# Kernel tuning notes

Hardware: AMD Instinct MI355X
Metric: run time of the kernel (lower is better)

The kernel has to match this reference:

```python
import jax, jax.numpy as jnp
import numpy as np

IN_CH = 32
OUT_CH = 32
HIDDEN = 32  # edge/angle MLP hidden width


def setup_inputs() -> dict:
    key = jax.random.key(0)
    ks = jax.random.split(key, 13)
    N, E, A = 50000, 200000, 400000
    s = 0.1
    return {
        "x": jax.random.normal(ks[0], (N, IN_CH), dtype=jnp.float32),
        "edge_index": jax.random.randint(ks[1], (2, E), 0, N),
        "edge_attr": jax.random.uniform(ks[2], (E, 1), dtype=jnp.float32),
        "angle_index": jax.random.randint(ks[3], (3, A), 0, N),
        "angles": jax.random.uniform(ks[4], (A, 1), dtype=jnp.float32),
        # edge_mlp: Linear(1,32) -> ReLU -> Linear(32, in*out)
        "eW1": jax.random.normal(ks[5], (1, HIDDEN), dtype=jnp.float32) * s,
        "eb1": jax.random.normal(ks[6], (HIDDEN,), dtype=jnp.float32) * s,
        "eW2": jax.random.normal(ks[7], (HIDDEN, IN_CH * OUT_CH), dtype=jnp.float32) * s,
        "eb2": jax.random.normal(ks[8], (IN_CH * OUT_CH,), dtype=jnp.float32) * s,
        # angle_mlp: Linear(1,32) -> ReLU -> Linear(32, out)
        "aW1": jax.random.normal(ks[9], (1, HIDDEN), dtype=jnp.float32) * s,
        "ab1": jax.random.normal(ks[10], (HIDDEN,), dtype=jnp.float32) * s,
        "aW2": jax.random.normal(ks[11], (HIDDEN, OUT_CH), dtype=jnp.float32) * s,
        "ab2": jax.random.normal(ks[12], (OUT_CH,), dtype=jnp.float32) * s,
    }


def reference(x, edge_index, edge_attr, angle_index, angles,
              eW1, eb1, eW2, eb2, aW1, ab1, aW2, ab2):
    N = x.shape[0]
    row, col = edge_index[0], edge_index[1]
    # per-edge weight matrices from edge MLP: (E, in, out)
    h = jax.nn.relu(edge_attr @ eW1 + eb1)
    edge_w = (h @ eW2 + eb2).reshape(-1, IN_CH, OUT_CH)
    # gather source node features, apply per-edge matrix (bmm)
    msg = jnp.einsum('ei,eio->eo', x[col], edge_w)  # (E, out)
    agg = jax.ops.segment_sum(msg, row, num_segments=N)
    # angle branch: scatter angle features onto center node j
    j = angle_index[1]
    angle_feat = jax.nn.relu(angles @ aW1 + ab1) @ aW2 + ab2  # (A, out)
    agg = agg + jax.ops.segment_sum(angle_feat, j, num_segments=N)
    return agg
```

## Files before the change

### kernel.cpp

```cpp
#include <hip/hip_runtime.h>
#include <hip/hip_bf16.h>
#include <stdint.h>

#define IC 32
#define OC 32
#define HID 32

#define PBIN 16
#define TSH 44
#define TSCALE 1048576.0f

#define PBE 12
#define MAXN 65536

typedef __attribute__((ext_vector_type(8))) _Float16 half8;
typedef __attribute__((ext_vector_type(4))) float f32x4;
typedef unsigned long long u64;

static __device__ __forceinline__ _Float16 f2h(float f) { return (_Float16)f; }

__device__ __align__(16) _Float16 g_MK[PBE * 2 * 32 * 32];
__device__ float g_ekn[16];
__device__ float g_akn[16];
__device__ int   g_npc[2];
__device__ __align__(16) u64 g_cells[(size_t)MAXN * PBIN];

__global__ __launch_bounds__(512) void setup_zero(
    const float* __restrict__ eW1, const float* __restrict__ eb1,
    const float* __restrict__ eW2, const float* __restrict__ eb2,
    const float* __restrict__ aW1, const float* __restrict__ ab1,
    float* __restrict__ out, int outF4, int cellF4)
{
    __shared__ float ts_s[32];
    __shared__ int   rk_s[32];
    __shared__ int   re_s[32];
    const int tid = threadIdx.x;
    const int bid = blockIdx.x;

    if (bid < 48) {
        if (bid == 0 && tid < 16) { g_ekn[tid] = 1e30f; g_akn[tid] = 1e30f; }
        if (tid < 32) {
            const int k = tid;
            const float w = eW1[k], b = eb1[k];
            const float ts = -b / w;
            const bool re = (w != 0.f) && (ts > 0.f) && (ts < 1.f);
            int rk = 0;
            for (int k2 = 0; k2 < 32; ++k2) {
                const float w2 = eW1[k2], b2 = eb1[k2];
                const float t2 = -b2 / w2;
                const bool re2 = (w2 != 0.f) && (t2 > 0.f) && (t2 < 1.f);
                rk += (re2 && (t2 < ts || (t2 == ts && k2 < k))) ? 1 : 0;
            }
            ts_s[k] = ts; rk_s[k] = rk; re_s[k] = re ? 1 : 0;
        }
        __syncthreads();

        if (bid == 0) {
            if (tid < 32) {
                if (re_s[tid]) g_ekn[rk_s[tid]] = ts_s[tid];
                if (tid == 0) {
                    int n = 0;
                    for (int k = 0; k < 32; ++k) n += re_s[k];
                    g_npc[0] = n + 1;
                }
            } else if (tid < 64) {
                const int k = tid - 32;
                const float w = aW1[k], b = ab1[k];
                const float ts = -b / w;
                const bool re = (w != 0.f) && (ts > 0.f) && (ts < 1.f);
                int rk = 0, nre = 0;
                for (int k2 = 0; k2 < 32; ++k2) {
                    const float w2 = aW1[k2], b2 = ab1[k2];
                    const float t2 = -b2 / w2;
                    const bool re2 = (w2 != 0.f) && (t2 > 0.f) && (t2 < 1.f);
                    nre += re2 ? 1 : 0;
                    rk += (re2 && (t2 < ts || (t2 == ts && k2 < k))) ? 1 : 0;
                }
                if (re) g_akn[rk] = ts;
                if (k == 0) g_npc[1] = nre + 1;
            }
        }

        const int gid = bid * 512 + tid;
        if (gid < PBE * 2 * 32 * 32) {
            const int i   = gid & 31;
            const int o   = (gid >> 5) & 31;
            const int mat = (gid >> 10) & 1;
            const int cc  = gid >> 11;
            float acc = (mat == 0) ? eb2[i * 32 + o] : 0.f;
            for (int k = 0; k < 32; ++k) {
                const bool flip = re_s[k] && (rk_s[k] < cc);
                const float w = eW1[k], b = eb1[k];
                const bool on0 = b > 0.f;
                const bool on = (w > 0.f) ? (on0 || flip) : (on0 && !flip);
                if (on) acc = fmaf((mat == 0 ? b : w),
                                   eW2[k * 1024 + i * 32 + o], acc);
            }
            g_MK[((cc * 2 + mat) * 32 + o) * 32 + i] = (_Float16)acc;
        }
    }

    const int total = outF4 + cellF4;
    const float4 z4 = make_float4(0.f, 0.f, 0.f, 0.f);
    for (int i = bid * 512 + tid; i < total; i += gridDim.x * 512) {
        if (i < outF4) ((float4*)out)[i] = z4;
        else           ((float4*)g_cells)[i - outF4] = z4;
    }
}

__global__ __launch_bounds__(256) void angle_scatter(
    const float* __restrict__ angles, const int* __restrict__ angle_index,
    u64* __restrict__ cells, int A)
{
    u64* cp = cells ? cells : g_cells;
    float kn[16];
#pragma unroll
    for (int j = 0; j < 16; ++j) kn[j] = g_akn[j];

    int i0 = blockIdx.x * blockDim.x + threadIdx.x;
    int stride = gridDim.x * blockDim.x;
    for (int a = i0; a < A; a += stride) {
        const float t = angles[a];
        const int j = angle_index[A + a];
        int cc = 0;
#pragma unroll
        for (int jj = 0; jj < 16; ++jj) cc += (t >= kn[jj]) ? 1 : 0;
        if ((unsigned)cc < (unsigned)PBIN) {
            const u64 enc = ((u64)1 << TSH) | (u64)(unsigned)(t * TSCALE);
            atomicAdd(cp + (size_t)j * PBIN + cc, enc);
        }
    }
}

static __device__ __forceinline__ void angle_gather_wave(
    const u64* __restrict__ cells, float* __restrict__ out,
    const float* __restrict__ aW1, const float* __restrict__ ab1,
    const float* __restrict__ aW2, const float* __restrict__ ab2,
    int N, int base, int lane, bool addmode)
{
    const int q = lane >> 4, l15 = lane & 15;
    float w1s[8], b1s[8];
    int c0 = 0, c1 = 0;
#pragma unroll
    for (int k = 0; k < HID; ++k) {
        const float w = aW1[k], b = ab1[k];
        const bool pos = w > 0.f;
        const bool f0 = pos ? (b > 0.f) : !(b > 0.f);
        const bool f1 = pos ? ((w + b) > 0.f) : !((w + b) > 0.f);
        c0 += f0 ? 1 : 0;
        c1 += f1 ? 1 : 0;
        if ((k >> 3) == q) { w1s[k & 7] = w; b1s[k & 7] = b; }
    }
    int npc = c1 - c0 + 1;
    if (npc > PBIN) npc = PBIN;

    half8 Bf0, Bf1;
#pragma unroll
    for (int j = 0; j < 8; ++j) {
        Bf0[j] = f2h(aW2[(q * 8 + j) * OC + l15]);
        Bf1[j] = f2h(aW2[(q * 8 + j) * OC + 16 + l15]);
    }
    const float bias0 = ab2[l15];
    const float bias1 = ab2[16 + l15];

    const int jn = base + l15;
    const bool vn = (jn < N);
    const u64* cj = cells + (size_t)(vn ? jn : 0) * PBIN;
    float g[8] = {0.f, 0.f, 0.f, 0.f, 0.f, 0.f, 0.f, 0.f};
    float tot = 0.f;
    for (int cc = 0; cc < npc; ++cc) {
        const u64 v = vn ? cj[cc] : 0;
        if (v) {
            const float n  = (float)(unsigned)(v >> TSH);
            const float ts = (float)(v & (((u64)1 << TSH) - 1)) * (1.f / TSCALE);
            const float tb = ts / n;
#pragma unroll
            for (int k = 0; k < 8; ++k) {
                float h = fmaf(tb, w1s[k], b1s[k]);
                h = h > 0.f ? h : 0.f;
                g[k] = fmaf(n, h, g[k]);
            }
            tot += n;
        }
    }
    half8 a;
#pragma unroll
    for (int k = 0; k < 8; ++k) a[k] = f2h(g[k]);

    f32x4 acc0 = {0.f, 0.f, 0.f, 0.f};
    f32x4 acc1 = {0.f, 0.f, 0.f, 0.f};
    acc0 = __builtin_amdgcn_mfma_f32_16x16x32_f16(a, Bf0, acc0, 0, 0, 0);
    acc1 = __builtin_amdgcn_mfma_f32_16x16x32_f16(a, Bf1, acc1, 0, 0, 0);

#pragma unroll
    for (int r = 0; r < 4; ++r) {
        const int node = base + q * 4 + r;
        const float tr = __shfl(tot, q * 4 + r, 64);
        if (node < N) {
            const float v0 = fmaf(tr, bias0, acc0[r]);
            const float v1 = fmaf(tr, bias1, acc1[r]);
            if (addmode) {
                unsafeAtomicAdd(out + (size_t)node * OC + l15, v0);
                unsafeAtomicAdd(out + (size_t)node * OC + 16 + l15, v1);
            } else {
                out[(size_t)node * OC + l15]      = v0;
                out[(size_t)node * OC + 16 + l15] = v1;
            }
        }
    }
}

__global__ __launch_bounds__(256) void angle_gather_ow(
    float* __restrict__ out,
    const float* __restrict__ aW1, const float* __restrict__ ab1,
    const float* __restrict__ aW2, const float* __restrict__ ab2, int N)
{
    const int lane = threadIdx.x & 63;
    const int wib  = threadIdx.x >> 6;
    const int base = (blockIdx.x * 4 + wib) * 16;
    if (base >= N) return;
    angle_gather_wave((const u64*)out, out, aW1, ab1, aW2, ab2,
                      N, base, lane, false);
}

__global__ __launch_bounds__(512, 4) void mega_kernel(
    const float* __restrict__ x, const int* __restrict__ edge_index,
    const float* __restrict__ edge_attr,
    const float* __restrict__ eW1, const float* __restrict__ eb1,
    const float* __restrict__ eW2, const float* __restrict__ eb2,
    const float* __restrict__ angles, const int* __restrict__ angle_index,
    const float* __restrict__ aW1, const float* __restrict__ ab1,
    const float* __restrict__ aW2, const float* __restrict__ ab2,
    float* __restrict__ out, int E, int A, int N,
    int EB, int GB, int FA, int FE)
{
    __shared__ __align__(16) _Float16 B[PBE * 2 * 32 * 32];
    __shared__ float knl[16];

    const int tid = threadIdx.x;
    const int bid = blockIdx.x;

    if (bid < EB) {
        for (int idx = tid; idx < PBE * 2 * 32 * 4; idx += 512) {
            const int r = idx >> 2;
            ((float4*)B)[idx ^ (r & 7)] = ((const float4*)g_MK)[idx];
        }
        if (tid < 16) knl[tid] = g_ekn[tid];
        __syncthreads();

        float kn[PBE];
#pragma unroll
        for (int j = 0; j < PBE; ++j) kn[j] = knl[j];
        int npc = g_npc[0];
        if (npc > PBE) npc = PBE;

        const int lane  = tid & 63;
        const int w8    = tid >> 6;
        const int gwave = bid * 8 + w8;
        const int ot    = gwave & 1;
        const int tile0 = gwave >> 1;
        const int tstride = (EB * 8) >> 1;
        const int q     = lane >> 4;
        const int l15   = lane & 15;
        const int ocol  = ot * 16 + l15;
        const int laneF4 = (ocol * 4 + q) ^ (ocol & 7);
        const _Float16* Bb = B + laneF4 * 8;
        const half8 z = {0, 0, 0, 0, 0, 0, 0, 0};

        const int numTiles = (E + 15) >> 4;

        for (int tile = tile0; tile < numTiles; tile += 2 * tstride) {
            const int tA = tile;
            const int tB = tile + tstride;
            const bool hasB = (tB < numTiles);

            const int eA  = (tA << 4) + l15;
            const bool va = (eA < E);
            const float ta = va ? edge_attr[eA] : 0.f;
            const int colA = va ? edge_index[E + eA] : 0;

            const int eB  = (tB << 4) + l15;
            const bool vb = hasB && (eB < E);
            const float tb = vb ? edge_attr[eB] : 0.f;
            const int colB = vb ? edge_index[E + eB] : 0;

            const float* xpA = x + (size_t)colA * IC + q * 8;
            const float4 xloA = *(const float4*)(xpA);
            const float4 xhiA = *(const float4*)(xpA + 4);
            const float* xpB = x + (size_t)colB * IC + q * 8;
            const float4 xloB = *(const float4*)(xpB);
            const float4 xhiB = *(const float4*)(xpB + 4);

            int dstsA[4], dstsB[4];
            const int ebaseA = (tA << 4) + q * 4;
            const int ebaseB = (tB << 4) + q * 4;
#pragma unroll
            for (int r = 0; r < 4; ++r) {
                const int erA = ebaseA + r;
                dstsA[r] = (erA < E) ? edge_index[erA] : -1;
                const int erB = ebaseB + r;
                dstsB[r] = (hasB && erB < E) ? edge_index[erB] : -1;
            }

            int ccA = 0, ccB = 0;
#pragma unroll
            for (int j = 0; j < PBE; ++j) {
                ccA += (ta >= kn[j]) ? 1 : 0;
                ccB += (tb >= kn[j]) ? 1 : 0;
            }

            half8 xhA, xhB;
            xhA[0] = f2h(xloA.x); xhA[1] = f2h(xloA.y);
            xhA[2] = f2h(xloA.z); xhA[3] = f2h(xloA.w);
            xhA[4] = f2h(xhiA.x); xhA[5] = f2h(xhiA.y);
            xhA[6] = f2h(xhiA.z); xhA[7] = f2h(xhiA.w);
            xhB[0] = f2h(xloB.x); xhB[1] = f2h(xloB.y);
            xhB[2] = f2h(xloB.z); xhB[3] = f2h(xloB.w);
            xhB[4] = f2h(xhiB.x); xhB[5] = f2h(xhiB.y);
            xhB[6] = f2h(xhiB.z); xhB[7] = f2h(xhiB.w);

            const _Float16 thA = f2h(ta), thB = f2h(tb);
            const half8 tvA = {thA, thA, thA, thA, thA, thA, thA, thA};
            const half8 tvB = {thB, thB, thB, thB, thB, thB, thB, thB};
            const half8 xtA = xhA * tvA;
            const half8 xtB = xhB * tvB;

            f32x4 accA = {0.f, 0.f, 0.f, 0.f};
            f32x4 accB = {0.f, 0.f, 0.f, 0.f};
            for (int c = 0; c < npc; ++c) {
                const half8 bM = *(const half8*)(Bb + (size_t)(c * 2 + 0) * 1024);
                const half8 bK = *(const half8*)(Bb + (size_t)(c * 2 + 1) * 1024);
                const half8 aA1 = (ccA == c) ? xhA : z;
                const half8 aA2 = (ccA == c) ? xtA : z;
                const half8 aB1 = (ccB == c) ? xhB : z;
                const half8 aB2 = (ccB == c) ? xtB : z;
                accA = __builtin_amdgcn_mfma_f32_16x16x32_f16(aA1, bM, accA, 0, 0, 0);
                accB = __builtin_amdgcn_mfma_f32_16x16x32_f16(aB1, bM, accB, 0, 0, 0);
                accA = __builtin_amdgcn_mfma_f32_16x16x32_f16(aA2, bK, accA, 0, 0, 0);
                accB = __builtin_amdgcn_mfma_f32_16x16x32_f16(aB2, bK, accB, 0, 0, 0);
            }

#pragma unroll
            for (int r = 0; r < 4; ++r) {
                if (dstsA[r] >= 0)
                    unsafeAtomicAdd(out + (size_t)dstsA[r] * OC + ocol, accA[r]);
            }
#pragma unroll
            for (int r = 0; r < 4; ++r) {
                if (dstsB[r] >= 0)
                    unsafeAtomicAdd(out + (size_t)dstsB[r] * OC + ocol, accB[r]);
            }
        }
    } else if (bid < EB + GB) {
        const int lane = tid & 63;
        const int wib  = tid >> 6;
        const int base = ((bid - EB) * 8 + wib) * 16;
        if (base < N)
            angle_gather_wave(g_cells, out, aW1, ab1, aW2, ab2,
                              N, base, lane, true);
    } else if (bid < EB + GB + FA) {
        if (g_npc[1] <= PBIN) return;
        const float kn15 = g_akn[15];
        float w1[HID], b1[HID];
#pragma unroll
        for (int k = 0; k < HID; ++k) { w1[k] = aW1[k]; b1[k] = ab1[k]; }
        int i0 = (bid - EB - GB) * 512 + tid;
        int stride = FA * 512;
        for (int a = i0; a < A; a += stride) {
            const float t = angles[a];
            if (t < kn15) continue;
            const int j = angle_index[A + a];
            float h[HID];
#pragma unroll
            for (int k = 0; k < HID; ++k) {
                float v = fmaf(t, w1[k], b1[k]);
                h[k] = v > 0.f ? v : 0.f;
            }
            for (int o = 0; o < OC; ++o) {
                float s = ab2[o];
#pragma unroll
                for (int k = 0; k < HID; ++k) s = fmaf(h[k], aW2[k * OC + o], s);
                unsafeAtomicAdd(out + (size_t)j * OC + o, s);
            }
        }
    } else {
        if (g_npc[0] <= PBE) return;
        const float knb = g_ekn[PBE - 1];
        int i0 = (bid - EB - GB - FA) * 512 + tid;
        int stride = FE * 512;
        for (int e = i0; e < E; e += stride) {
            const float t = edge_attr[e];
            if (t < knb) continue;
            const int col = edge_index[E + e];
            const int dst = edge_index[e];
            float h[HID];
#pragma unroll
            for (int k = 0; k < HID; ++k) {
                float v = fmaf(t, eW1[k], eb1[k]);
                h[k] = v > 0.f ? v : 0.f;
            }
            for (int o = 0; o < OC; ++o) {
                float s = 0.f;
                for (int i = 0; i < IC; ++i) {
                    float wio = eb2[i * 32 + o];
#pragma unroll
                    for (int k = 0; k < HID; ++k)
                        wio = fmaf(h[k], eW2[k * 1024 + i * 32 + o], wio);
                    s = fmaf(x[(size_t)col * IC + i], wio, s);
                }
                unsafeAtomicAdd(out + (size_t)dst * OC + o, s);
            }
        }
    }
}

extern "C" void kernel_launch(void* const* d_in, const int* in_sizes, int n_in,
                              void* d_out, int out_size, void* d_ws, size_t ws_size,
                              hipStream_t stream)
{
    const float* x          = (const float*)d_in[0];
    const int*   edge_index = (const int*)d_in[1];
    const float* edge_attr  = (const float*)d_in[2];
    const int*   angle_index= (const int*)d_in[3];
    const float* angles     = (const float*)d_in[4];
    const float* eW1        = (const float*)d_in[5];
    const float* eb1        = (const float*)d_in[6];
    const float* eW2        = (const float*)d_in[7];
    const float* eb2        = (const float*)d_in[8];
    const float* aW1        = (const float*)d_in[9];
    const float* ab1        = (const float*)d_in[10];
    const float* aW2        = (const float*)d_in[11];
    const float* ab2        = (const float*)d_in[12];
    float* out = (float*)d_out;
    (void)d_ws; (void)ws_size;

    const int E = in_sizes[1] / 2;
    const int A = in_sizes[3] / 3;
    const int N = in_sizes[0] / IC;

    const int outF4 = out_size / 4;
    const int sblocks = (A + 255) / 256;

    if (N <= MAXN) {
        const int cellF4 = N * 8;
        int zg = (outF4 + cellF4 + 511) / 512;
        if (zg < 48) zg = 48;
        setup_zero<<<zg, 512, 0, stream>>>(eW1, eb1, eW2, eb2, aW1, ab1,
                                           out, outF4, cellF4);

        angle_scatter<<<sblocks, 256, 0, stream>>>(angles, angle_index,
                                                   nullptr, A);

        const int EB = 768;
        const int GB = (N + 127) / 128;
        const int FA = 64, FE = 64;
        mega_kernel<<<EB + GB + FA + FE, 512, 0, stream>>>(
            x, edge_index, edge_attr, eW1, eb1, eW2, eb2,
            angles, angle_index, aW1, ab1, aW2, ab2,
            out, E, A, N, EB, GB, FA, FE);
    } else {
        int zg = (outF4 + 511) / 512;
        if (zg < 48) zg = 48;
        setup_zero<<<zg, 512, 0, stream>>>(eW1, eb1, eW2, eb2, aW1, ab1,
                                           out, outF4, 0);
        angle_scatter<<<sblocks, 256, 0, stream>>>(angles, angle_index,
                                                   (u64*)out, A);
        angle_gather_ow<<<(N + 63) / 64, 256, 0, stream>>>(out, aW1, ab1,
                                                           aW2, ab2, N);
        const int EB = 768, FA = 64, FE = 64;
        mega_kernel<<<EB + FA + FE, 512, 0, stream>>>(
            x, edge_index, edge_attr, eW1, eb1, eW2, eb2,
            angles, angle_index, aW1, ab1, aW2, ab2,
            out, E, A, N, EB, 0, FA, FE);
    }
}
```

Baseline: 157.1 us.

## Bucket edges by piecewise segment so each tile runs one MFMA pair

Edges are now counting-sorted by their ReLU-piecewise segment inside angle_scatter, which writes packed (t, col, row) entries into per-segment workspace buckets. The edge phase of mega_kernel then walks tiles that each belong to a single segment and issues only one pair of MFMAs per tile, instead of looping over every segment with masked inputs. This removes redundant MFMA and LDS work, at the cost of an extra pass over edges with global atomics, 64-bit workspace traffic, and quantizing edge_attr to 20 bits. The old path is kept as a fallback when the workspace is too small or E is too large.

```diff
diff --git a/kernel.cpp b/kernel.cpp
--- a/kernel.cpp
+++ b/kernel.cpp
@@ -12,6 +12,7 @@
 
 #define PBE 12
 #define MAXN 65536
+#define MAXEB (1 << 18)
 
 typedef __attribute__((ext_vector_type(8))) _Float16 half8;
 typedef __attribute__((ext_vector_type(4))) float f32x4;
@@ -24,6 +25,7 @@
 __device__ float g_akn[16];
 __device__ int   g_npc[2];
 __device__ __align__(16) u64 g_cells[(size_t)MAXN * PBIN];
+__device__ unsigned g_bpos[PBE];
 
 __global__ __launch_bounds__(512) void setup_zero(
     const float* __restrict__ eW1, const float* __restrict__ eb1,
@@ -37,8 +39,11 @@
     const int tid = threadIdx.x;
     const int bid = blockIdx.x;
 
+    if (bid == 0 && tid < PBE) g_bpos[tid] = 0u;
+
     if (bid < 48) {
-        if (bid == 0 && tid < 16) { g_ekn[tid] = 1e30f; g_akn[tid] = 1e30f; }
+        if (bid == 0 && tid >= 16 && tid < 32) { g_ekn[tid-16] = 1e30f; g_akn[tid-16] = 1e30f; }
+        __syncthreads();
         if (tid < 32) {
             const int k = tid;
             const float w = eW1[k], b = eb1[k];
@@ -110,15 +115,24 @@
 
 __global__ __launch_bounds__(256) void angle_scatter(
     const float* __restrict__ angles, const int* __restrict__ angle_index,
-    u64* __restrict__ cells, int A)
+    const float* __restrict__ edge_attr, const int* __restrict__ edge_index,
+    u64* __restrict__ cells, u64* __restrict__ sorted,
+    int A, int E, int doSort)
 {
+    __shared__ unsigned hist[PBE], basePB[PBE], pos2[PBE];
+
     u64* cp = cells ? cells : g_cells;
     float kn[16];
 #pragma unroll
     for (int j = 0; j < 16; ++j) kn[j] = g_akn[j];
-
-    int i0 = blockIdx.x * blockDim.x + threadIdx.x;
-    int stride = gridDim.x * blockDim.x;
+    float ek[PBE];
+#pragma unroll
+    for (int j = 0; j < PBE; ++j) ek[j] = g_ekn[j];
+
+    const int tid = threadIdx.x;
+    const int i0 = blockIdx.x * blockDim.x + tid;
+    const int stride = gridDim.x * blockDim.x;
+
     for (int a = i0; a < A; a += stride) {
         const float t = angles[a];
         const int j = angle_index[A + a];
@@ -128,6 +142,44 @@
         if ((unsigned)cc < (unsigned)PBIN) {
             const u64 enc = ((u64)1 << TSH) | (u64)(unsigned)(t * TSCALE);
             atomicAdd(cp + (size_t)j * PBIN + cc, enc);
+        }
+    }
+
+    if (doSort) {
+        const int nb = gridDim.x;
+        const int chunk = (E + nb - 1) / nb;
+        const int e0 = blockIdx.x * chunk;
+        int e1 = e0 + chunk;
+        if (e1 > E) e1 = E;
+
+        if (tid < PBE) { hist[tid] = 0u; pos2[tid] = 0u; }
+        __syncthreads();
+
+        for (int e = e0 + tid; e < e1; e += blockDim.x) {
+            const float t = edge_attr[e];
+            int cc = 0;
+#pragma unroll
+            for (int j = 0; j < PBE; ++j) cc += (t >= ek[j]) ? 1 : 0;
+            if (cc < PBE) atomicAdd(&hist[cc], 1u);
+        }
+        __syncthreads();
+        if (tid < PBE) basePB[tid] = atomicAdd(&g_bpos[tid], hist[tid]);
+        __syncthreads();
+
+        for (int e = e0 + tid; e < e1; e += blockDim.x) {
+            const float t = edge_attr[e];
+            int cc = 0;
+#pragma unroll
+            for (int j = 0; j < PBE; ++j) cc += (t >= ek[j]) ? 1 : 0;
+            if (cc < PBE) {
+                const unsigned lp = atomicAdd(&pos2[cc], 1u);
+                unsigned tq = (unsigned)(t * TSCALE);
+                if (tq > 1048575u) tq = 1048575u;
+                const u64 ent = ((u64)tq << 44)
+                              | ((u64)(unsigned)edge_index[E + e] << 22)
+                              | (u64)(unsigned)edge_index[e];
+                sorted[(size_t)cc * MAXEB + basePB[cc] + lp] = ent;
+            }
         }
     }
 }
@@ -231,8 +283,9 @@
     const float* __restrict__ angles, const int* __restrict__ angle_index,
     const float* __restrict__ aW1, const float* __restrict__ ab1,
     const float* __restrict__ aW2, const float* __restrict__ ab2,
+    const u64* __restrict__ sorted,
     float* __restrict__ out, int E, int A, int N,
-    int EB, int GB, int FA, int FE)
+    int EB, int GB, int FA, int FE, int useSort)
 {
     __shared__ __align__(16) _Float16 B[PBE * 2 * 32 * 32];
     __shared__ float knl[16];
@@ -247,12 +300,6 @@
         }
         if (tid < 16) knl[tid] = g_ekn[tid];
         __syncthreads();
-
-        float kn[PBE];
-#pragma unroll
-        for (int j = 0; j < PBE; ++j) kn[j] = knl[j];
-        int npc = g_npc[0];
-        if (npc > PBE) npc = PBE;
 
         const int lane  = tid & 63;
         const int w8    = tid >> 6;
@@ -267,88 +314,190 @@
         const _Float16* Bb = B + laneF4 * 8;
         const half8 z = {0, 0, 0, 0, 0, 0, 0, 0};
 
-        const int numTiles = (E + 15) >> 4;
-
-        for (int tile = tile0; tile < numTiles; tile += 2 * tstride) {
-            const int tA = tile;
-            const int tB = tile + tstride;
-            const bool hasB = (tB < numTiles);
-
-            const int eA  = (tA << 4) + l15;
-            const bool va = (eA < E);
-            const float ta = va ? edge_attr[eA] : 0.f;
-            const int colA = va ? edge_index[E + eA] : 0;
-
-            const int eB  = (tB << 4) + l15;
-            const bool vb = hasB && (eB < E);
-            const float tb = vb ? edge_attr[eB] : 0.f;
-            const int colB = vb ? edge_index[E + eB] : 0;
-
-            const float* xpA = x + (size_t)colA * IC + q * 8;
-            const float4 xloA = *(const float4*)(xpA);
-            const float4 xhiA = *(const float4*)(xpA + 4);
-            const float* xpB = x + (size_t)colB * IC + q * 8;
-            const float4 xloB = *(const float4*)(xpB);
-            const float4 xhiB = *(const float4*)(xpB + 4);
-
-            int dstsA[4], dstsB[4];
-            const int ebaseA = (tA << 4) + q * 4;
-            const int ebaseB = (tB << 4) + q * 4;
-#pragma unroll
-            for (int r = 0; r < 4; ++r) {
-                const int erA = ebaseA + r;
-                dstsA[r] = (erA < E) ? edge_index[erA] : -1;
-                const int erB = ebaseB + r;
-                dstsB[r] = (hasB && erB < E) ? edge_index[erB] : -1;
-            }
-
-            int ccA = 0, ccB = 0;
-#pragma unroll
-            for (int j = 0; j < PBE; ++j) {
-                ccA += (ta >= kn[j]) ? 1 : 0;
-                ccB += (tb >= kn[j]) ? 1 : 0;
-            }
-
-            half8 xhA, xhB;
-            xhA[0] = f2h(xloA.x); xhA[1] = f2h(xloA.y);
-            xhA[2] = f2h(xloA.z); xhA[3] = f2h(xloA.w);
-            xhA[4] = f2h(xhiA.x); xhA[5] = f2h(xhiA.y);
-            xhA[6] = f2h(xhiA.z); xhA[7] = f2h(xhiA.w);
-            xhB[0] = f2h(xloB.x); xhB[1] = f2h(xloB.y);
-            xhB[2] = f2h(xloB.z); xhB[3] = f2h(xloB.w);
-            xhB[4] = f2h(xhiB.x); xhB[5] = f2h(xhiB.y);
-            xhB[6] = f2h(xhiB.z); xhB[7] = f2h(xhiB.w);
-
-            const _Float16 thA = f2h(ta), thB = f2h(tb);
-            const half8 tvA = {thA, thA, thA, thA, thA, thA, thA, thA};
-            const half8 tvB = {thB, thB, thB, thB, thB, thB, thB, thB};
-            const half8 xtA = xhA * tvA;
-            const half8 xtB = xhB * tvB;
-
-            f32x4 accA = {0.f, 0.f, 0.f, 0.f};
-            f32x4 accB = {0.f, 0.f, 0.f, 0.f};
-            for (int c = 0; c < npc; ++c) {
-                const half8 bM = *(const half8*)(Bb + (size_t)(c * 2 + 0) * 1024);
-                const half8 bK = *(const half8*)(Bb + (size_t)(c * 2 + 1) * 1024);
-                const half8 aA1 = (ccA == c) ? xhA : z;
-                const half8 aA2 = (ccA == c) ? xtA : z;
-                const half8 aB1 = (ccB == c) ? xhB : z;
-                const half8 aB2 = (ccB == c) ? xtB : z;
-                accA = __builtin_amdgcn_mfma_f32_16x16x32_f16(aA1, bM, accA, 0, 0, 0);
-                accB = __builtin_amdgcn_mfma_f32_16x16x32_f16(aB1, bM, accB, 0, 0, 0);
-                accA = __builtin_amdgcn_mfma_f32_16x16x32_f16(aA2, bK, accA, 0, 0, 0);
-                accB = __builtin_amdgcn_mfma_f32_16x16x32_f16(aB2, bK, accB, 0, 0, 0);
-            }
-
-#pragma unroll
-            for (int r = 0; r < 4; ++r) {
-                if (dstsA[r] >= 0)
-                    unsafeAtomicAdd(out + (size_t)dstsA[r] * OC + ocol, accA[r]);
-            }
-#pragma unroll
-            for (int r = 0; r < 4; ++r) {
-                if (dstsB[r] >= 0)
-                    unsafeAtomicAdd(out + (size_t)dstsB[r] * OC + ocol, accB[r]);
+        if (useSort) {
+            unsigned cnt[PBE];
+            int pfx[PBE + 1];
+            pfx[0] = 0;
+#pragma unroll
+            for (int c = 0; c < PBE; ++c) {
+                cnt[c] = g_bpos[c];
+                pfx[c + 1] = pfx[c] + (int)((cnt[c] + 15u) >> 4);
+            }
+            const int totTiles = pfx[PBE];
+
+            for (int v = tile0; v < totTiles; v += 2 * tstride) {
+                const int vA = v;
+                const int vB = v + tstride;
+                const bool hasB = (vB < totTiles);
+
+                int cA = 0, pbA = 0; unsigned cnA = cnt[0];
+                int cB = 0, pbB = 0; unsigned cnB = cnt[0];
+#pragma unroll
+                for (int c = 1; c < PBE; ++c) {
+                    const bool gA = (vA >= pfx[c]);
+                    const bool gB = (vB >= pfx[c]);
+                    cA += gA ? 1 : 0;  pbA = gA ? pfx[c] : pbA;
+                    cnA = gA ? cnt[c] : cnA;
+                    cB += gB ? 1 : 0;  pbB = gB ? pfx[c] : pbB;
+                    cnB = gB ? cnt[c] : cnB;
+                }
+                const int iA = (vA - pbA) * 16 + l15;
+                const int iB = (vB - pbB) * 16 + l15;
+                const bool va = (unsigned)iA < cnA;
+                const bool vb = hasB && ((unsigned)iB < cnB);
+
+                const u64 entA = va ? sorted[(size_t)cA * MAXEB + iA] : 0;
+                const u64 entB = vb ? sorted[(size_t)cB * MAXEB + iB] : 0;
+
+                const float ta = (float)(unsigned)(entA >> 44) * (1.f / TSCALE);
+                const float tb = (float)(unsigned)(entB >> 44) * (1.f / TSCALE);
+                const int colA = (int)((entA >> 22) & 0x3FFFFFu);
+                const int colB = (int)((entB >> 22) & 0x3FFFFFu);
+                const int dA_self = va ? (int)(entA & 0x3FFFFFu) : -1;
+                const int dB_self = vb ? (int)(entB & 0x3FFFFFu) : -1;
+
+                const float* xpA = x + (size_t)colA * IC + q * 8;
+                const float4 xloA = *(const float4*)(xpA);
+                const float4 xhiA = *(const float4*)(xpA + 4);
+                const float* xpB = x + (size_t)colB * IC + q * 8;
+                const float4 xloB = *(const float4*)(xpB);
+                const float4 xhiB = *(const float4*)(xpB + 4);
+
+                int dstsA[4], dstsB[4];
+#pragma unroll
+                for (int r = 0; r < 4; ++r) {
+                    dstsA[r] = __shfl(dA_self, q * 4 + r, 64);
+                    dstsB[r] = __shfl(dB_self, q * 4 + r, 64);
+                }
+
+                const half8 bMA = *(const half8*)(Bb + (size_t)(cA * 2 + 0) * 1024);
+                const half8 bKA = *(const half8*)(Bb + (size_t)(cA * 2 + 1) * 1024);
+                const half8 bMB = *(const half8*)(Bb + (size_t)(cB * 2 + 0) * 1024);
+                const half8 bKB = *(const half8*)(Bb + (size_t)(cB * 2 + 1) * 1024);
+
+                half8 xhA, xhB;
+                xhA[0] = f2h(xloA.x); xhA[1] = f2h(xloA.y);
+                xhA[2] = f2h(xloA.z); xhA[3] = f2h(xloA.w);
+                xhA[4] = f2h(xhiA.x); xhA[5] = f2h(xhiA.y);
+                xhA[6] = f2h(xhiA.z); xhA[7] = f2h(xhiA.w);
+                xhB[0] = f2h(xloB.x); xhB[1] = f2h(xloB.y);
+                xhB[2] = f2h(xloB.z); xhB[3] = f2h(xloB.w);
+                xhB[4] = f2h(xhiB.x); xhB[5] = f2h(xhiB.y);
+                xhB[6] = f2h(xhiB.z); xhB[7] = f2h(xhiB.w);
+
+                const _Float16 thA = f2h(ta), thB = f2h(tb);
+                const half8 tvA = {thA, thA, thA, thA, thA, thA, thA, thA};
+                const half8 tvB = {thB, thB, thB, thB, thB, thB, thB, thB};
+                const half8 xtA = xhA * tvA;
+                const half8 xtB = xhB * tvB;
+
+                f32x4 accA = {0.f, 0.f, 0.f, 0.f};
+                f32x4 accB = {0.f, 0.f, 0.f, 0.f};
+                accA = __builtin_amdgcn_mfma_f32_16x16x32_f16(xhA, bMA, accA, 0, 0, 0);
+                accB = __builtin_amdgcn_mfma_f32_16x16x32_f16(xhB, bMB, accB, 0, 0, 0);
+                accA = __builtin_amdgcn_mfma_f32_16x16x32_f16(xtA, bKA, accA, 0, 0, 0);
+                accB = __builtin_amdgcn_mfma_f32_16x16x32_f16(xtB, bKB, accB, 0, 0, 0);
+
+#pragma unroll
+                for (int r = 0; r < 4; ++r) {
+                    if (dstsA[r] >= 0)
+                        unsafeAtomicAdd(out + (size_t)dstsA[r] * OC + ocol, accA[r]);
+                }
+#pragma unroll
+                for (int r = 0; r < 4; ++r) {
+                    if (dstsB[r] >= 0)
+                        unsafeAtomicAdd(out + (size_t)dstsB[r] * OC + ocol, accB[r]);
+                }
+            }
+        } else {
+            float kn[PBE];
+#pragma unroll
+            for (int j = 0; j < PBE; ++j) kn[j] = knl[j];
+            int npc = g_npc[0];
+            if (npc > PBE) npc = PBE;
+
+            const int numTiles = (E + 15) >> 4;
+            for (int tile = tile0; tile < numTiles; tile += 2 * tstride) {
+                const int tA = tile;
+                const int tB = tile + tstride;
+                const bool hasB = (tB < numTiles);
+
+                const int eA  = (tA << 4) + l15;
+                const bool va = (eA < E);
+                const float ta = va ? edge_attr[eA] : 0.f;
+                const int colA = va ? edge_index[E + eA] : 0;
+
+                const int eB  = (tB << 4) + l15;
+                const bool vb = hasB && (eB < E);
+                const float tb = vb ? edge_attr[eB] : 0.f;
+                const int colB = vb ? edge_index[E + eB] : 0;
+
+                const float* xpA = x + (size_t)colA * IC + q * 8;
+                const float4 xloA = *(const float4*)(xpA);
+                const float4 xhiA = *(const float4*)(xpA + 4);
+                const float* xpB = x + (size_t)colB * IC + q * 8;
+                const float4 xloB = *(const float4*)(xpB);
+                const float4 xhiB = *(const float4*)(xpB + 4);
+
+                int dstsA[4], dstsB[4];
+                const int ebaseA = (tA << 4) + q * 4;
+                const int ebaseB = (tB << 4) + q * 4;
+#pragma unroll
+                for (int r = 0; r < 4; ++r) {
+                    const int erA = ebaseA + r;
+                    dstsA[r] = (erA < E) ? edge_index[erA] : -1;
+                    const int erB = ebaseB + r;
+                    dstsB[r] = (hasB && erB < E) ? edge_index[erB] : -1;
+                }
+
+                int ccA = 0, ccB = 0;
+#pragma unroll
+                for (int j = 0; j < PBE; ++j) {
+                    ccA += (ta >= kn[j]) ? 1 : 0;
+                    ccB += (tb >= kn[j]) ? 1 : 0;
+                }
+
+                half8 xhA, xhB;
+                xhA[0] = f2h(xloA.x); xhA[1] = f2h(xloA.y);
+                xhA[2] = f2h(xloA.z); xhA[3] = f2h(xloA.w);
+                xhA[4] = f2h(xhiA.x); xhA[5] = f2h(xhiA.y);
+                xhA[6] = f2h(xhiA.z); xhA[7] = f2h(xhiA.w);
+                xhB[0] = f2h(xloB.x); xhB[1] = f2h(xloB.y);
+                xhB[2] = f2h(xloB.z); xhB[3] = f2h(xloB.w);
+                xhB[4] = f2h(xhiB.x); xhB[5] = f2h(xhiB.y);
+                xhB[6] = f2h(xhiB.z); xhB[7] = f2h(xhiB.w);
+
+                const _Float16 thA = f2h(ta), thB = f2h(tb);
+                const half8 tvA = {thA, thA, thA, thA, thA, thA, thA, thA};
+                const half8 tvB = {thB, thB, thB, thB, thB, thB, thB, thB};
+                const half8 xtA = xhA * tvA;
+                const half8 xtB = xhB * tvB;
+
+                f32x4 accA = {0.f, 0.f, 0.f, 0.f};
+                f32x4 accB = {0.f, 0.f, 0.f, 0.f};
+                for (int c = 0; c < npc; ++c) {
+                    const half8 bM = *(const half8*)(Bb + (size_t)(c * 2 + 0) * 1024);
+                    const half8 bK = *(const half8*)(Bb + (size_t)(c * 2 + 1) * 1024);
+                    const half8 aA1 = (ccA == c) ? xhA : z;
+                    const half8 aA2 = (ccA == c) ? xtA : z;
+                    const half8 aB1 = (ccB == c) ? xhB : z;
+                    const half8 aB2 = (ccB == c) ? xtB : z;
+                    accA = __builtin_amdgcn_mfma_f32_16x16x32_f16(aA1, bM, accA, 0, 0, 0);
+                    accB = __builtin_amdgcn_mfma_f32_16x16x32_f16(aB1, bM, accB, 0, 0, 0);
+                    accA = __builtin_amdgcn_mfma_f32_16x16x32_f16(aA2, bK, accA, 0, 0, 0);
+                    accB = __builtin_amdgcn_mfma_f32_16x16x32_f16(aB2, bK, accB, 0, 0, 0);
+                }
+
+#pragma unroll
+                for (int r = 0; r < 4; ++r) {
+                    if (dstsA[r] >= 0)
+                        unsafeAtomicAdd(out + (size_t)dstsA[r] * OC + ocol, accA[r]);
+                }
+#pragma unroll
+                for (int r = 0; r < 4; ++r) {
+                    if (dstsB[r] >= 0)
+                        unsafeAtomicAdd(out + (size_t)dstsB[r] * OC + ocol, accB[r]);
+                }
             }
         }
     } else if (bid < EB + GB) {
@@ -432,45 +581,65 @@
     const float* aW2        = (const float*)d_in[11];
     const float* ab2        = (const float*)d_in[12];
     float* out = (float*)d_out;
-    (void)d_ws; (void)ws_size;
 
     const int E = in_sizes[1] / 2;
     const int A = in_sizes[3] / 3;
     const int N = in_sizes[0] / IC;
 
     const int outF4 = out_size / 4;
-    const int sblocks = (A + 255) / 256;
-
-    if (N <= MAXN) {
+    const size_t sortBytes = (size_t)PBE * MAXEB * sizeof(u64);
+    const bool fast = (N <= MAXN) && (E <= MAXEB) &&
+                      (d_ws != nullptr) && (ws_size >= sortBytes);
+    u64* sorted = (u64*)d_ws;
+
+    if (fast) {
         const int cellF4 = N * 8;
         int zg = (outF4 + cellF4 + 511) / 512;
         if (zg < 48) zg = 48;
         setup_zero<<<zg, 512, 0, stream>>>(eW1, eb1, eW2, eb2, aW1, ab1,
                                            out, outF4, cellF4);
 
-        angle_scatter<<<sblocks, 256, 0, stream>>>(angles, angle_index,
-                                                   nullptr, A);
+        angle_scatter<<<512, 256, 0, stream>>>(angles, angle_index,
+                                               edge_attr, edge_index,
+                                               nullptr, sorted, A, E, 1);
 
         const int EB = 768;
         const int GB = (N + 127) / 128;
         const int FA = 64, FE = 64;
         mega_kernel<<<EB + GB + FA + FE, 512, 0, stream>>>(
             x, edge_index, edge_attr, eW1, eb1, eW2, eb2,
-            angles, angle_index, aW1, ab1, aW2, ab2,
-            out, E, A, N, EB, GB, FA, FE);
+            angles, angle_index, aW1, ab1, aW2, ab2, sorted,
+            out, E, A, N, EB, GB, FA, FE, 1);
+    } else if (N <= MAXN) {
+        const int cellF4 = N * 8;
+        int zg = (outF4 + cellF4 + 511) / 512;
+        if (zg < 48) zg = 48;
+        setup_zero<<<zg, 512, 0, stream>>>(eW1, eb1, eW2, eb2, aW1, ab1,
+                                           out, outF4, cellF4);
+        angle_scatter<<<512, 256, 0, stream>>>(angles, angle_index,
+                                               edge_attr, edge_index,
+                                               nullptr, nullptr, A, E, 0);
+        const int EB = 768;
+        const int GB = (N + 127) / 128;
+        const int FA = 64, FE = 64;
+        mega_kernel<<<EB + GB + FA + FE, 512, 0, stream>>>(
+            x, edge_index, edge_attr, eW1, eb1, eW2, eb2,
+            angles, angle_index, aW1, ab1, aW2, ab2, nullptr,
+            out, E, A, N, EB, GB, FA, FE, 0);
     } else {
         int zg = (outF4 + 511) / 512;
         if (zg < 48) zg = 48;
         setup_zero<<<zg, 512, 0, stream>>>(eW1, eb1, eW2, eb2, aW1, ab1,
                                            out, outF4, 0);
-        angle_scatter<<<sblocks, 256, 0, stream>>>(angles, angle_index,
-                                                   (u64*)out, A);
+        angle_scatter<<<512, 256, 0, stream>>>(angles, angle_index,
+                                               edge_attr, edge_index,
+                                               (u64*)out, nullptr, A, E, 0);
         angle_gather_ow<<<(N + 63) / 64, 256, 0, stream>>>(out, aW1, ab1,
                                                            aW2, ab2, N);
         const int EB = 768, FA = 64, FE = 64;
         mega_kernel<<<EB + FA + FE, 512, 0, stream>>>(
             x, edge_index, edge_attr, eW1, eb1, eW2, eb2,
-            angles, angle_index, aW1, ab1, aW2, ab2,
-            out, E, A, N, EB, 0, FA, FE);
+            angles, angle_index, aW1, ab1, aW2, ab2, nullptr,
+            out, E, A, N, EB, 0, FA, FE, 0);
     }
 }
```

Result: slower. 160.4 us (+2.1%).
